# Performance work log

Measured on AMD Instinct MI355X. Metric: run time of the kernel, lower is better.

## Reference

```python
import jax, jax.numpy as jnp
import numpy as np

N, E = 50000, 1600000
DIM_IN, HEADS, DIM_OUT = 256, 4, 32
NEG_SLOPE = 0.2


def setup_inputs() -> dict:
    key = jax.random.key(0)
    k1, k2, k3, k4, k5, k6 = jax.random.split(key, 6)
    x = jax.random.normal(k1, (N, DIM_IN), dtype=jnp.float32)
    edge_index = jax.random.randint(k2, (2, E), 0, N, dtype=jnp.int64)
    s = 1.0 / np.sqrt(DIM_IN)
    W = jax.random.normal(k3, (DIM_IN, HEADS * DIM_OUT), dtype=jnp.float32) * s
    att_src = jax.random.normal(k4, (HEADS, DIM_OUT), dtype=jnp.float32) * 0.1
    att_dst = jax.random.normal(k5, (HEADS, DIM_OUT), dtype=jnp.float32) * 0.1
    bias = jax.random.normal(k6, (HEADS * DIM_OUT,), dtype=jnp.float32) * 0.01
    return {"x": x, "edge_index": edge_index, "W": W,
            "att_src": att_src, "att_dst": att_dst, "bias": bias}


def reference(x, edge_index, W, att_src, att_dst, bias):
    n = x.shape[0]
    h, c = att_src.shape
    # linear projection, per-head view [N, H, C]
    xp = (x @ W).reshape(n, h, c)
    # per-node attention logits [N, H]
    a_src = jnp.einsum('nhc,hc->nh', xp, att_src)
    a_dst = jnp.einsum('nhc,hc->nh', xp, att_dst)
    # add self loops (PyG default add_self_loops=True)
    loops = jnp.arange(n, dtype=edge_index.dtype)
    src = jnp.concatenate([edge_index[0], loops])  # [E+N]
    dst = jnp.concatenate([edge_index[1], loops])
    # edge attention scores [E+N, H]
    e = jax.nn.leaky_relu(a_src[src] + a_dst[dst], negative_slope=NEG_SLOPE)
    # segment softmax over incoming edges of each dst node
    emax = jax.ops.segment_max(e, dst, num_segments=n)
    ex = jnp.exp(e - emax[dst])
    denom = jax.ops.segment_sum(ex, dst, num_segments=n)
    alpha = ex / denom[dst]  # [E+N, H]
    # weighted scatter-aggregate of src features
    msg = xp[src] * alpha[:, :, None]  # [E+N, H, C]
    out = jax.ops.segment_sum(msg, dst, num_segments=n)  # [N, H, C]
    return out.reshape(n, h * c) + bias
```

## Files before the change

### kernel.cpp

```cpp
#include <hip/hip_runtime.h>
#include <hip/hip_fp16.h>


#define DIN 256
#define HC 128
#define NH 4
#define NEG 0.2f
#define BSH 8
#define BSZ 256

typedef _Float16 half8 __attribute__((ext_vector_type(8)));
typedef _Float16 half2v __attribute__((ext_vector_type(2)));
typedef float f32x4 __attribute__((ext_vector_type(4)));

__global__ __launch_bounds__(256) void wtrans_kernel(const float* __restrict__ W,
                                                     _Float16* __restrict__ Wt,
                                                     int* __restrict__ ghist) {
    int i = blockIdx.x * 256 + threadIdx.x;
    if (i < 257) ghist[i] = 0;
    int k = i >> 7, c = i & 127;
    Wt[c * 256 + k] = (_Float16)W[i];
}

__global__ __launch_bounds__(256) void proj_kernel(const float* __restrict__ x,
                                                   const _Float16* __restrict__ Wt,
                                                   const float* __restrict__ attS,
                                                   const float* __restrict__ attD,
                                                   __half* __restrict__ xph,
                                                   float* __restrict__ a_src,
                                                   float* __restrict__ a_dst, int n) {
    __shared__ _Float16 smem[8704];
    __shared__ float attSL[128], attDL[128];
    _Float16* xs = smem;
    _Float16* Wl = smem + 2560;
    _Float16* ep = smem;

    const int tid  = threadIdx.x;
    const int node0 = blockIdx.x * 64;
    const int wave = tid >> 6;
    const int lane = tid & 63;
    const int l15  = lane & 15;
    const int quad = lane >> 4;

    if (tid < 128) attSL[tid] = attS[tid];
    else           attDL[tid - 128] = attD[tid - 128];

    f32x4 acc[8];
#pragma unroll
    for (int ct = 0; ct < 8; ++ct) acc[ct] = (f32x4){0.f, 0.f, 0.f, 0.f};

    for (int kt = 0; kt < DIN; kt += 32) {
        __syncthreads();
#pragma unroll
        for (int r = 0; r < 4; ++r) {
            int idx = tid + r * 256;
            int row = idx >> 4;
            int kp  = idx & 15;
            int gn = node0 + row;
            float2 xv = make_float2(0.f, 0.f);
            if (gn < n) xv = *(const float2*)&x[(size_t)gn * DIN + kt + kp * 2];
            half2v p; p[0] = (_Float16)xv.x; p[1] = (_Float16)xv.y;
            *(half2v*)&xs[row * 40 + kp * 2] = p;
        }
#pragma unroll
        for (int r = 0; r < 2; ++r) {
            int id = tid + r * 256;
            int c = id >> 2;
            int q = id & 3;
            half8 wv = *(const half8*)&Wt[(size_t)c * 256 + kt + q * 8];
            *(half8*)&Wl[c * 40 + q * 8] = wv;
        }
        __syncthreads();
        half8 af = *(const half8*)&xs[(wave * 16 + l15) * 40 + quad * 8];
#pragma unroll
        for (int ct = 0; ct < 8; ++ct) {
            half8 bf = *(const half8*)&Wl[(ct * 16 + l15) * 40 + quad * 8];
            acc[ct] = __builtin_amdgcn_mfma_f32_16x16x32_f16(af, bf, acc[ct], 0, 0, 0);
        }
    }
    __syncthreads();
#pragma unroll
    for (int ct = 0; ct < 8; ++ct)
#pragma unroll
        for (int r = 0; r < 4; ++r) {
            int row = wave * 16 + quad * 4 + r;
            ep[row * 136 + ct * 16 + l15] = (_Float16)acc[ct][r];
        }
    __syncthreads();
    {
        int row = tid >> 2, ch = tid & 3;
        int node = node0 + row;
        if (node < n) {
            const uint4* s = (const uint4*)&ep[row * 136 + ch * 32];
            uint4* d = (uint4*)&xph[(size_t)node * HC + ch * 32];
            d[0] = s[0]; d[1] = s[1]; d[2] = s[2]; d[3] = s[3];
        }
    }
    {
        int nl = tid >> 2, h = tid & 3;
        int node = node0 + nl;
        if (node < n) {
            float ps = 0.f, pd = 0.f;
            const _Float16* er = &ep[nl * 136 + h * 32];
#pragma unroll
            for (int c = 0; c < 32; ++c) {
                float v = (float)er[c];
                ps += v * attSL[h * 32 + c];
                pd += v * attDL[h * 32 + c];
            }
            a_src[node * NH + h] = ps;
            a_dst[node * NH + h] = pd;
        }
    }
}

__global__ __launch_bounds__(256) void hist_kernel(const int* __restrict__ ei,
                                                   int* __restrict__ ghist, int e, int n) {
    __shared__ int h[256];
    const int tid = threadIdx.x;
    h[tid] = 0;
    __syncthreads();
    const int base = blockIdx.x * 4096;
#pragma unroll
    for (int j = 0; j < 16; ++j) {
        int i = base + j * 256 + tid;
        if (i < e) {
            int dst = ei[e + i];
            if ((unsigned)dst < (unsigned)n) atomicAdd(&h[dst >> BSH], 1);
        }
    }
    __syncthreads();
    if (h[tid]) atomicAdd(&ghist[tid], h[tid]);
}

__global__ __launch_bounds__(256) void bscan_kernel(const int* __restrict__ ghist,
                                                    int* __restrict__ gbase,
                                                    int* __restrict__ gcur, int nbuck) {
    __shared__ int buf[256];
    const int tid = threadIdx.x;
    int v = (tid < nbuck) ? ghist[tid] : 0;
    buf[tid] = v;
    __syncthreads();
    for (int s = 1; s < 256; s <<= 1) {
        int t = (tid >= s) ? buf[tid - s] : 0;
        __syncthreads();
        buf[tid] += t;
        __syncthreads();
    }
    int excl = buf[tid] - v;
    if (tid < nbuck) { gbase[tid] = excl; gcur[tid] = excl; }
    if (tid == nbuck - 1) gbase[nbuck] = buf[tid];
}

__global__ __launch_bounds__(256) void bin_kernel(const int* __restrict__ ei,
                                                  int* __restrict__ gcur,
                                                  unsigned* __restrict__ binned,
                                                  int e, int n) {
    __shared__ int h[256];
    __shared__ int rbase[256];
    const int tid = threadIdx.x;
    h[tid] = 0;
    __syncthreads();
    const int base = blockIdx.x * 4096;
    unsigned pk[16];
    int bk[16];
#pragma unroll
    for (int j = 0; j < 16; ++j) {
        int i = base + j * 256 + tid;
        bk[j] = -1;
        if (i < e) {
            int src = ei[i];
            int dst = ei[e + i];
            if ((unsigned)dst < (unsigned)n && (unsigned)src < (unsigned)n) {
                bk[j] = dst >> BSH;
                pk[j] = ((unsigned)(dst & (BSZ - 1)) << 24) | (unsigned)src;
                atomicAdd(&h[bk[j]], 1);
            }
        }
    }
    __syncthreads();
    if (h[tid]) rbase[tid] = atomicAdd(&gcur[tid], h[tid]);
    h[tid] = 0;
    __syncthreads();
#pragma unroll
    for (int j = 0; j < 16; ++j) {
        if (bk[j] >= 0) {
            int p = atomicAdd(&h[bk[j]], 1);
            binned[rbase[bk[j]] + p] = pk[j];
        }
    }
}

__global__ __launch_bounds__(1024) void csr_kernel(const unsigned* __restrict__ binned,
                                                   const int* __restrict__ gbase,
                                                   int* __restrict__ off,
                                                   unsigned* __restrict__ srt,
                                                   int n, int nbuck) {
    __shared__ int cnt[256], buf[256], cur[256];
    const int tid = threadIdx.x;
    const int b = blockIdx.x;
    const int kb = gbase[b];
    const int ke = gbase[b + 1];
    if (tid < 256) cnt[tid] = 0;
    __syncthreads();
    for (int i = kb + tid; i < ke; i += 1024)
        atomicAdd(&cnt[binned[i] >> 24], 1);
    __syncthreads();
    int v = 0;
    if (tid < 256) { v = cnt[tid]; buf[tid] = v; }
    __syncthreads();
    for (int s = 1; s < 256; s <<= 1) {
        int t = (tid < 256 && tid >= s) ? buf[tid - s] : 0;
        __syncthreads();
        if (tid < 256) buf[tid] += t;
        __syncthreads();
    }
    if (tid < 256) {
        const int excl = kb + buf[tid] - v;
        const int node = b * BSZ + tid;
        if (node < n) off[node] = excl;
        if (tid == 0 && b == nbuck - 1) off[n] = ke;
        cur[tid] = excl;
    }
    __syncthreads();
    const unsigned dbase = (unsigned)(b * BSZ) << 16;
    for (int i = kb + tid; i < ke; i += 1024) {
        unsigned pv = binned[i];
        int nl = pv >> 24;
        int pos = atomicAdd(&cur[nl], 1);
        srt[pos] = (dbase + ((unsigned)nl << 16)) | (pv & 0xFFFFu);
    }
}

__global__ __launch_bounds__(256) void escore_kernel(const unsigned* __restrict__ srt,
                                                     const float* __restrict__ a_src,
                                                     const float* __restrict__ a_dst,
                                                     __half* __restrict__ escore,
                                                     int e, int n) {
    int i = blockIdx.x * 256 + threadIdx.x;
    if (i >= e) return;
    unsigned v = srt[i];
    int src = (int)(v & 0xFFFFu);
    int dst = (int)(v >> 16);
    if (src >= n || dst >= n) return;
    const float4 as = *(const float4*)&a_src[(size_t)src * 4];
    const float4 ad = *(const float4*)&a_dst[(size_t)dst * 4];
    float t0 = as.x + ad.x; t0 = (t0 > 0.f) ? t0 : NEG * t0;
    float t1 = as.y + ad.y; t1 = (t1 > 0.f) ? t1 : NEG * t1;
    float t2 = as.z + ad.z; t2 = (t2 > 0.f) ? t2 : NEG * t2;
    float t3 = as.w + ad.w; t3 = (t3 > 0.f) ? t3 : NEG * t3;
    __half2* ep = (__half2*)&escore[(size_t)i * 4];
    ep[0] = __floats2half2_rn(__expf(t0), __expf(t1));
    ep[1] = __floats2half2_rn(__expf(t2), __expf(t3));
}

__global__ __launch_bounds__(256) void agg_kernel(const __half* __restrict__ xph,
                                                  const float* __restrict__ a_src,
                                                  const float* __restrict__ a_dst,
                                                  const int* __restrict__ off,
                                                  const unsigned* __restrict__ srt,
                                                  const __half* __restrict__ escore,
                                                  const float* __restrict__ bias,
                                                  float* __restrict__ out, int n) {
    const int gwave = (blockIdx.x * blockDim.x + threadIdx.x) >> 6;
    if (gwave >= n) return;
    const int node = gwave;
    const int lane = threadIdx.x & 63;
    const int g = lane >> 4;
    const int l = lane & 15;
    const int h = l >> 2;

    float acc[8];
#pragma unroll
    for (int c = 0; c < 8; ++c) acc[c] = 0.f;
    float den = 0.f;

    if (g == 0) {
        float e0 = a_src[node * NH + h] + a_dst[node * NH + h];
        e0 = (e0 > 0.f) ? e0 : NEG * e0;
        float sl = __expf(e0);
        half8 xv = *(const half8*)&xph[(size_t)node * HC + l * 8];
#pragma unroll
        for (int c = 0; c < 8; ++c) acc[c] = sl * (float)xv[c];
        den = sl;
    }

    const int kb = off[node];
    const int ke = off[node + 1];
    int k0 = kb;
    for (; k0 + 16 <= ke; k0 += 16) {
        const int kg = k0 + g * 4;
        unsigned sv[4];
        float sc[4];
        half8 hv[4];
#pragma unroll
        for (int j = 0; j < 4; ++j) sv[j] = srt[kg + j];
#pragma unroll
        for (int j = 0; j < 4; ++j)
            hv[j] = *(const half8*)&xph[(size_t)(sv[j] & 0xFFFFu) * HC + l * 8];
#pragma unroll
        for (int j = 0; j < 4; ++j)
            sc[j] = __half2float(escore[(size_t)(kg + j) * 4 + h]);
#pragma unroll
        for (int j = 0; j < 4; ++j) {
            const float s = sc[j];
#pragma unroll
            for (int c = 0; c < 8; ++c) acc[c] += s * (float)hv[j][c];
            den += s;
        }
    }
    for (int k = k0 + g; k < ke; k += 4) {
        const unsigned v = srt[k];
        const float s = __half2float(escore[(size_t)k * 4 + h]);
        const half8 hv = *(const half8*)&xph[(size_t)(v & 0xFFFFu) * HC + l * 8];
#pragma unroll
        for (int c = 0; c < 8; ++c) acc[c] += s * (float)hv[c];
        den += s;
    }

#pragma unroll
    for (int c = 0; c < 8; ++c) acc[c] += __shfl_xor(acc[c], 16, 64);
    den += __shfl_xor(den, 16, 64);
#pragma unroll
    for (int c = 0; c < 8; ++c) acc[c] += __shfl_xor(acc[c], 32, 64);
    den += __shfl_xor(den, 32, 64);

    if (lane < 16) {
        const float inv = 1.0f / den;
        const float4* b4 = (const float4*)&bias[l * 8];
        float4 o0, o1;
        o0.x = acc[0] * inv + b4[0].x;
        o0.y = acc[1] * inv + b4[0].y;
        o0.z = acc[2] * inv + b4[0].z;
        o0.w = acc[3] * inv + b4[0].w;
        o1.x = acc[4] * inv + b4[1].x;
        o1.y = acc[5] * inv + b4[1].y;
        o1.z = acc[6] * inv + b4[1].z;
        o1.w = acc[7] * inv + b4[1].w;
        float4* d = (float4*)&out[(size_t)node * HC + l * 8];
        d[0] = o0;
        d[1] = o1;
    }
}

extern "C" void kernel_launch(void* const* d_in, const int* in_sizes, int n_in,
                              void* d_out, int out_size, void* d_ws, size_t ws_size,
                              hipStream_t stream) {
    if (n_in < 6 || !d_out || !d_ws) return;
    const float* x    = (const float*)d_in[0];
    const int*   ei   = (const int*)d_in[1];
    const float* W    = (const float*)d_in[2];
    const float* attS = (const float*)d_in[3];
    const float* attD = (const float*)d_in[4];
    const float* bias = (const float*)d_in[5];
    float* out = (float*)d_out;

    const int N = in_sizes[0] / DIN;
    const int E = in_sizes[1] / 2;
    if (N <= 0 || E <= 0) return;
    const int NBUCK = (N + BSZ - 1) >> BSH;
    if (NBUCK > 256 || N > 65536) return;

    char* ws = (char*)d_ws;
    size_t off_b = 0;
    auto carve = [&](size_t bytes) {
        size_t p = off_b;
        off_b = (off_b + bytes + 255) & ~(size_t)255;
        return (void*)(ws + p);
    };
    __half*    xph    = (__half*)carve((size_t)N * HC * 2);
    _Float16*  Wt     = (_Float16*)carve((size_t)HC * DIN * 2);
    float*     a_src  = (float*)carve((size_t)N * NH * 4);
    float*     a_dst  = (float*)carve((size_t)N * NH * 4);
    int*       ghist  = (int*)carve(257 * 4);
    int*       gbase  = (int*)carve(257 * 4);
    int*       gcur   = (int*)carve(257 * 4);
    unsigned*  binned = (unsigned*)carve((size_t)E * 4);
    int*       offp   = (int*)carve((size_t)(N + 1) * 4);
    unsigned*  srt    = (unsigned*)carve((size_t)E * 4);
    __half*    escore = (__half*)carve((size_t)E * NH * 2);
    (void)out_size;
    if (off_b > ws_size) return;

    const int ECH = (E + 4095) / 4096;

    wtrans_kernel<<<(DIN * HC) / 256, 256, 0, stream>>>(W, Wt, ghist);
    proj_kernel<<<(N + 63) / 64, 256, 0, stream>>>(x, Wt, attS, attD, (__half*)xph, a_src, a_dst, N);
    hist_kernel<<<ECH, 256, 0, stream>>>(ei, ghist, E, N);
    bscan_kernel<<<1, 256, 0, stream>>>(ghist, gbase, gcur, NBUCK);
    bin_kernel<<<ECH, 256, 0, stream>>>(ei, gcur, binned, E, N);
    csr_kernel<<<NBUCK, 1024, 0, stream>>>(binned, gbase, offp, srt, N, NBUCK);
    escore_kernel<<<(E + 255) / 256, 256, 0, stream>>>(srt, a_src, a_dst, escore, E, N);
    agg_kernel<<<(N * 64 + 255) / 256, 256, 0, stream>>>(xph, a_src, a_dst,
                                                         offp, srt, escore, bias, out, N);
}
```

Baseline: 240.6 us.

## Merge preprocessing kernels, overlap projection with binning, recompute edge scores in aggregation

Cuts the kernel chain from eight launches to five. Histogram runs alongside the weight transpose, the bucket scan is recomputed per block instead of in its own launch, and the projection is split across the binning and CSR launches so independent work shares the GPU. The separate edge-score kernel and its fp16 escore buffer are gone: aggregation now gathers a_src per edge and computes exp(leaky_relu) inline. The sorted index array shrinks to 16-bit source ids. This trades redundant per-block scans and extra gathers and exp work in aggregation for fewer launches and less global memory traffic.

New measurement: 233.4 us. 1.03x faster.

```diff
diff --git a/kernel.cpp b/kernel.cpp
--- a/kernel.cpp
+++ b/kernel.cpp
@@ -13,30 +13,25 @@
 typedef _Float16 half2v __attribute__((ext_vector_type(2)));
 typedef float f32x4 __attribute__((ext_vector_type(4)));
 
-__global__ __launch_bounds__(256) void wtrans_kernel(const float* __restrict__ W,
-                                                     _Float16* __restrict__ Wt,
-                                                     int* __restrict__ ghist) {
-    int i = blockIdx.x * 256 + threadIdx.x;
-    if (i < 257) ghist[i] = 0;
-    int k = i >> 7, c = i & 127;
-    Wt[c * 256 + k] = (_Float16)W[i];
-}
-
-__global__ __launch_bounds__(256) void proj_kernel(const float* __restrict__ x,
-                                                   const _Float16* __restrict__ Wt,
-                                                   const float* __restrict__ attS,
-                                                   const float* __restrict__ attD,
-                                                   __half* __restrict__ xph,
-                                                   float* __restrict__ a_src,
-                                                   float* __restrict__ a_dst, int n) {
-    __shared__ _Float16 smem[8704];
-    __shared__ float attSL[128], attDL[128];
-    _Float16* xs = smem;
-    _Float16* Wl = smem + 2560;
-    _Float16* ep = smem;
+__global__ void zero_kernel(int* __restrict__ p, int n) {
+    int i = blockIdx.x * blockDim.x + threadIdx.x;
+    if (i < n) p[i] = 0;
+}
+
+__device__ __forceinline__ void proj_body(char* sm, const float* __restrict__ x,
+                                          const _Float16* __restrict__ Wt,
+                                          const float* __restrict__ attS,
+                                          const float* __restrict__ attD,
+                                          __half* __restrict__ xph,
+                                          float* __restrict__ a_src,
+                                          float* __restrict__ a_dst, int n, int node0) {
+    _Float16* xs = (_Float16*)sm;
+    _Float16* Wl = (_Float16*)(sm + 5120);
+    _Float16* ep = (_Float16*)sm;
+    float* attSL = (float*)(sm + 17408);
+    float* attDL = (float*)(sm + 17920);
 
     const int tid  = threadIdx.x;
-    const int node0 = blockIdx.x * 64;
     const int wave = tid >> 6;
     const int lane = tid & 63;
     const int l15  = lane & 15;
@@ -114,152 +109,163 @@
     }
 }
 
-__global__ __launch_bounds__(256) void hist_kernel(const int* __restrict__ ei,
-                                                   int* __restrict__ ghist, int e, int n) {
-    __shared__ int h[256];
-    const int tid = threadIdx.x;
-    h[tid] = 0;
-    __syncthreads();
-    const int base = blockIdx.x * 4096;
-#pragma unroll
-    for (int j = 0; j < 16; ++j) {
-        int i = base + j * 256 + tid;
-        if (i < e) {
-            int dst = ei[e + i];
-            if ((unsigned)dst < (unsigned)n) atomicAdd(&h[dst >> BSH], 1);
-        }
-    }
-    __syncthreads();
-    if (h[tid]) atomicAdd(&ghist[tid], h[tid]);
-}
-
-__global__ __launch_bounds__(256) void bscan_kernel(const int* __restrict__ ghist,
-                                                    int* __restrict__ gbase,
-                                                    int* __restrict__ gcur, int nbuck) {
-    __shared__ int buf[256];
-    const int tid = threadIdx.x;
-    int v = (tid < nbuck) ? ghist[tid] : 0;
-    buf[tid] = v;
-    __syncthreads();
-    for (int s = 1; s < 256; s <<= 1) {
-        int t = (tid >= s) ? buf[tid - s] : 0;
-        __syncthreads();
-        buf[tid] += t;
-        __syncthreads();
-    }
-    int excl = buf[tid] - v;
-    if (tid < nbuck) { gbase[tid] = excl; gcur[tid] = excl; }
-    if (tid == nbuck - 1) gbase[nbuck] = buf[tid];
-}
-
-__global__ __launch_bounds__(256) void bin_kernel(const int* __restrict__ ei,
-                                                  int* __restrict__ gcur,
+__global__ __launch_bounds__(256) void k_hist_wtrans(const int* __restrict__ ei,
+                                                     int* __restrict__ ghist,
+                                                     const float* __restrict__ W,
+                                                     _Float16* __restrict__ Wt,
+                                                     int e, int n, int ech) {
+    if ((int)blockIdx.x < ech) {
+        __shared__ int h[256];
+        const int tid = threadIdx.x;
+        h[tid] = 0;
+        __syncthreads();
+        const int base = blockIdx.x * 4096;
+#pragma unroll
+        for (int j = 0; j < 16; ++j) {
+            int i = base + j * 256 + tid;
+            if (i < e) {
+                int dst = ei[e + i];
+                if ((unsigned)dst < (unsigned)n) atomicAdd(&h[dst >> BSH], 1);
+            }
+        }
+        __syncthreads();
+        if (h[tid]) atomicAdd(&ghist[tid], h[tid]);
+    } else {
+        int i = ((int)blockIdx.x - ech) * 256 + threadIdx.x;
+        int k = i >> 7, c = i & 127;
+        Wt[c * 256 + k] = (_Float16)W[i];
+    }
+}
+
+__global__ __launch_bounds__(256) void k_bin_proj(const int* __restrict__ ei,
+                                                  const int* __restrict__ ghist,
+                                                  int* __restrict__ gcur0,
                                                   unsigned* __restrict__ binned,
-                                                  int e, int n) {
-    __shared__ int h[256];
-    __shared__ int rbase[256];
-    const int tid = threadIdx.x;
-    h[tid] = 0;
-    __syncthreads();
-    const int base = blockIdx.x * 4096;
-    unsigned pk[16];
-    int bk[16];
-#pragma unroll
-    for (int j = 0; j < 16; ++j) {
-        int i = base + j * 256 + tid;
-        bk[j] = -1;
-        if (i < e) {
-            int src = ei[i];
-            int dst = ei[e + i];
-            if ((unsigned)dst < (unsigned)n && (unsigned)src < (unsigned)n) {
-                bk[j] = dst >> BSH;
-                pk[j] = ((unsigned)(dst & (BSZ - 1)) << 24) | (unsigned)src;
-                atomicAdd(&h[bk[j]], 1);
+                                                  const float* __restrict__ x,
+                                                  const _Float16* __restrict__ Wt,
+                                                  const float* __restrict__ attS,
+                                                  const float* __restrict__ attD,
+                                                  __half* __restrict__ xph,
+                                                  float* __restrict__ a_src,
+                                                  float* __restrict__ a_dst,
+                                                  int e, int n, int ech) {
+    __shared__ __attribute__((aligned(16))) char sm[18432];
+    if ((int)blockIdx.x < ech) {
+        int* h     = (int*)sm;
+        int* rbase = (int*)(sm + 1024);
+        int* buf   = (int*)(sm + 2048);
+        const int tid = threadIdx.x;
+        const int gh = ghist[tid];
+        buf[tid] = gh;
+        h[tid] = 0;
+        __syncthreads();
+        for (int s = 1; s < 256; s <<= 1) {
+            int t = (tid >= s) ? buf[tid - s] : 0;
+            __syncthreads();
+            buf[tid] += t;
+            __syncthreads();
+        }
+        const int gbase_t = buf[tid] - gh;
+        const int base = blockIdx.x * 4096;
+        unsigned pk[16];
+        int bk[16];
+#pragma unroll
+        for (int j = 0; j < 16; ++j) {
+            int i = base + j * 256 + tid;
+            bk[j] = -1;
+            if (i < e) {
+                int src = ei[i];
+                int dst = ei[e + i];
+                if ((unsigned)dst < (unsigned)n && (unsigned)src < (unsigned)n) {
+                    bk[j] = dst >> BSH;
+                    pk[j] = ((unsigned)(dst & (BSZ - 1)) << 24) | (unsigned)src;
+                    atomicAdd(&h[bk[j]], 1);
+                }
             }
         }
-    }
-    __syncthreads();
-    if (h[tid]) rbase[tid] = atomicAdd(&gcur[tid], h[tid]);
-    h[tid] = 0;
-    __syncthreads();
-#pragma unroll
-    for (int j = 0; j < 16; ++j) {
-        if (bk[j] >= 0) {
-            int p = atomicAdd(&h[bk[j]], 1);
-            binned[rbase[bk[j]] + p] = pk[j];
-        }
-    }
-}
-
-__global__ __launch_bounds__(1024) void csr_kernel(const unsigned* __restrict__ binned,
-                                                   const int* __restrict__ gbase,
-                                                   int* __restrict__ off,
-                                                   unsigned* __restrict__ srt,
-                                                   int n, int nbuck) {
-    __shared__ int cnt[256], buf[256], cur[256];
-    const int tid = threadIdx.x;
-    const int b = blockIdx.x;
-    const int kb = gbase[b];
-    const int ke = gbase[b + 1];
-    if (tid < 256) cnt[tid] = 0;
-    __syncthreads();
-    for (int i = kb + tid; i < ke; i += 1024)
-        atomicAdd(&cnt[binned[i] >> 24], 1);
-    __syncthreads();
-    int v = 0;
-    if (tid < 256) { v = cnt[tid]; buf[tid] = v; }
-    __syncthreads();
-    for (int s = 1; s < 256; s <<= 1) {
-        int t = (tid < 256 && tid >= s) ? buf[tid - s] : 0;
-        __syncthreads();
-        if (tid < 256) buf[tid] += t;
-        __syncthreads();
-    }
-    if (tid < 256) {
+        __syncthreads();
+        if (h[tid]) rbase[tid] = gbase_t + atomicAdd(&gcur0[tid], h[tid]);
+        h[tid] = 0;
+        __syncthreads();
+#pragma unroll
+        for (int j = 0; j < 16; ++j) {
+            if (bk[j] >= 0) {
+                int p = atomicAdd(&h[bk[j]], 1);
+                binned[rbase[bk[j]] + p] = pk[j];
+            }
+        }
+    } else {
+        proj_body(sm, x, Wt, attS, attD, xph, a_src, a_dst, n, ((int)blockIdx.x - ech) * 64);
+    }
+}
+
+__global__ __launch_bounds__(256) void k_csr_proj(const unsigned* __restrict__ binned,
+                                                  const int* __restrict__ ghist,
+                                                  int* __restrict__ off,
+                                                  unsigned short* __restrict__ srt,
+                                                  const float* __restrict__ x,
+                                                  const _Float16* __restrict__ Wt,
+                                                  const float* __restrict__ attS,
+                                                  const float* __restrict__ attD,
+                                                  __half* __restrict__ xph,
+                                                  float* __restrict__ a_src,
+                                                  float* __restrict__ a_dst,
+                                                  int n, int nbuck, int pb1) {
+    __shared__ __attribute__((aligned(16))) char sm[18432];
+    if ((int)blockIdx.x < nbuck) {
+        int* cnt = (int*)sm;
+        int* buf = (int*)(sm + 1024);
+        int* cur = (int*)(sm + 2048);
+        const int tid = threadIdx.x;
+        const int b = blockIdx.x;
+        buf[tid] = ghist[tid];
+        __syncthreads();
+        for (int s = 1; s < 256; s <<= 1) {
+            int t = (tid >= s) ? buf[tid - s] : 0;
+            __syncthreads();
+            buf[tid] += t;
+            __syncthreads();
+        }
+        const int ke = buf[b];
+        const int kb = ke - ghist[b];
+        __syncthreads();
+        cnt[tid] = 0;
+        __syncthreads();
+        for (int i = kb + tid; i < ke; i += 256)
+            atomicAdd(&cnt[binned[i] >> 24], 1);
+        __syncthreads();
+        int v = cnt[tid];
+        buf[tid] = v;
+        __syncthreads();
+        for (int s = 1; s < 256; s <<= 1) {
+            int t = (tid >= s) ? buf[tid - s] : 0;
+            __syncthreads();
+            buf[tid] += t;
+            __syncthreads();
+        }
         const int excl = kb + buf[tid] - v;
         const int node = b * BSZ + tid;
         if (node < n) off[node] = excl;
         if (tid == 0 && b == nbuck - 1) off[n] = ke;
         cur[tid] = excl;
-    }
-    __syncthreads();
-    const unsigned dbase = (unsigned)(b * BSZ) << 16;
-    for (int i = kb + tid; i < ke; i += 1024) {
-        unsigned pv = binned[i];
-        int nl = pv >> 24;
-        int pos = atomicAdd(&cur[nl], 1);
-        srt[pos] = (dbase + ((unsigned)nl << 16)) | (pv & 0xFFFFu);
-    }
-}
-
-__global__ __launch_bounds__(256) void escore_kernel(const unsigned* __restrict__ srt,
-                                                     const float* __restrict__ a_src,
-                                                     const float* __restrict__ a_dst,
-                                                     __half* __restrict__ escore,
-                                                     int e, int n) {
-    int i = blockIdx.x * 256 + threadIdx.x;
-    if (i >= e) return;
-    unsigned v = srt[i];
-    int src = (int)(v & 0xFFFFu);
-    int dst = (int)(v >> 16);
-    if (src >= n || dst >= n) return;
-    const float4 as = *(const float4*)&a_src[(size_t)src * 4];
-    const float4 ad = *(const float4*)&a_dst[(size_t)dst * 4];
-    float t0 = as.x + ad.x; t0 = (t0 > 0.f) ? t0 : NEG * t0;
-    float t1 = as.y + ad.y; t1 = (t1 > 0.f) ? t1 : NEG * t1;
-    float t2 = as.z + ad.z; t2 = (t2 > 0.f) ? t2 : NEG * t2;
-    float t3 = as.w + ad.w; t3 = (t3 > 0.f) ? t3 : NEG * t3;
-    __half2* ep = (__half2*)&escore[(size_t)i * 4];
-    ep[0] = __floats2half2_rn(__expf(t0), __expf(t1));
-    ep[1] = __floats2half2_rn(__expf(t2), __expf(t3));
+        __syncthreads();
+        for (int i = kb + tid; i < ke; i += 256) {
+            unsigned pv = binned[i];
+            int nl = pv >> 24;
+            int pos = atomicAdd(&cur[nl], 1);
+            srt[pos] = (unsigned short)(pv & 0xFFFFu);
+        }
+    } else {
+        proj_body(sm, x, Wt, attS, attD, xph, a_src, a_dst, n,
+                  (pb1 + (int)blockIdx.x - nbuck) * 64);
+    }
 }
 
 __global__ __launch_bounds__(256) void agg_kernel(const __half* __restrict__ xph,
                                                   const float* __restrict__ a_src,
                                                   const float* __restrict__ a_dst,
                                                   const int* __restrict__ off,
-                                                  const unsigned* __restrict__ srt,
-                                                  const __half* __restrict__ escore,
+                                                  const unsigned short* __restrict__ srt,
                                                   const float* __restrict__ bias,
                                                   float* __restrict__ out, int n) {
     const int gwave = (blockIdx.x * blockDim.x + threadIdx.x) >> 6;
@@ -270,19 +276,21 @@
     const int l = lane & 15;
     const int h = l >> 2;
 
+    const float ad = a_dst[node * NH + h];
+
     float acc[8];
 #pragma unroll
     for (int c = 0; c < 8; ++c) acc[c] = 0.f;
     float den = 0.f;
 
     if (g == 0) {
-        float e0 = a_src[node * NH + h] + a_dst[node * NH + h];
-        e0 = (e0 > 0.f) ? e0 : NEG * e0;
-        float sl = __expf(e0);
+        float t = a_src[node * NH + h] + ad;
+        t = fmaxf(t, 0.f) + NEG * fminf(t, 0.f);
+        float s = __expf(t);
         half8 xv = *(const half8*)&xph[(size_t)node * HC + l * 8];
 #pragma unroll
-        for (int c = 0; c < 8; ++c) acc[c] = sl * (float)xv[c];
-        den = sl;
+        for (int c = 0; c < 8; ++c) acc[c] = s * (float)xv[c];
+        den = s;
     }
 
     const int kb = off[node];
@@ -290,29 +298,32 @@
     int k0 = kb;
     for (; k0 + 16 <= ke; k0 += 16) {
         const int kg = k0 + g * 4;
-        unsigned sv[4];
-        float sc[4];
+        int sv[4];
+        float asv[4];
         half8 hv[4];
 #pragma unroll
         for (int j = 0; j < 4; ++j) sv[j] = srt[kg + j];
 #pragma unroll
+        for (int j = 0; j < 4; ++j) asv[j] = a_src[sv[j] * NH + h];
+#pragma unroll
         for (int j = 0; j < 4; ++j)
-            hv[j] = *(const half8*)&xph[(size_t)(sv[j] & 0xFFFFu) * HC + l * 8];
-#pragma unroll
-        for (int j = 0; j < 4; ++j)
-            sc[j] = __half2float(escore[(size_t)(kg + j) * 4 + h]);
+            hv[j] = *(const half8*)&xph[(size_t)sv[j] * HC + l * 8];
 #pragma unroll
         for (int j = 0; j < 4; ++j) {
-            const float s = sc[j];
+            float t = asv[j] + ad;
+            t = fmaxf(t, 0.f) + NEG * fminf(t, 0.f);
+            const float s = __expf(t);
 #pragma unroll
             for (int c = 0; c < 8; ++c) acc[c] += s * (float)hv[j][c];
             den += s;
         }
     }
     for (int k = k0 + g; k < ke; k += 4) {
-        const unsigned v = srt[k];
-        const float s = __half2float(escore[(size_t)k * 4 + h]);
-        const half8 hv = *(const half8*)&xph[(size_t)(v & 0xFFFFu) * HC + l * 8];
+        const int sv = srt[k];
+        float t = a_src[sv * NH + h] + ad;
+        t = fmaxf(t, 0.f) + NEG * fminf(t, 0.f);
+        const float s = __expf(t);
+        const half8 hv = *(const half8*)&xph[(size_t)sv * HC + l * 8];
 #pragma unroll
         for (int c = 0; c < 8; ++c) acc[c] += s * (float)hv[c];
         den += s;
@@ -368,29 +379,32 @@
         off_b = (off_b + bytes + 255) & ~(size_t)255;
         return (void*)(ws + p);
     };
-    __half*    xph    = (__half*)carve((size_t)N * HC * 2);
-    _Float16*  Wt     = (_Float16*)carve((size_t)HC * DIN * 2);
-    float*     a_src  = (float*)carve((size_t)N * NH * 4);
-    float*     a_dst  = (float*)carve((size_t)N * NH * 4);
-    int*       ghist  = (int*)carve(257 * 4);
-    int*       gbase  = (int*)carve(257 * 4);
-    int*       gcur   = (int*)carve(257 * 4);
-    unsigned*  binned = (unsigned*)carve((size_t)E * 4);
-    int*       offp   = (int*)carve((size_t)(N + 1) * 4);
-    unsigned*  srt    = (unsigned*)carve((size_t)E * 4);
-    __half*    escore = (__half*)carve((size_t)E * NH * 2);
+    __half*         xph    = (__half*)carve((size_t)N * HC * 2);
+    _Float16*       Wt     = (_Float16*)carve((size_t)HC * DIN * 2);
+    float*          a_src  = (float*)carve((size_t)N * NH * 4);
+    float*          a_dst  = (float*)carve((size_t)N * NH * 4);
+    int*            gz     = (int*)carve(512 * 4);
+    unsigned*       binned = (unsigned*)carve((size_t)E * 4);
+    int*            offp   = (int*)carve((size_t)(N + 1) * 4);
+    unsigned short* srt    = (unsigned short*)carve((size_t)E * 2);
     (void)out_size;
     if (off_b > ws_size) return;
 
+    int* ghist = gz;
+    int* gcur0 = gz + 256;
+
     const int ECH = (E + 4095) / 4096;
-
-    wtrans_kernel<<<(DIN * HC) / 256, 256, 0, stream>>>(W, Wt, ghist);
-    proj_kernel<<<(N + 63) / 64, 256, 0, stream>>>(x, Wt, attS, attD, (__half*)xph, a_src, a_dst, N);
-    hist_kernel<<<ECH, 256, 0, stream>>>(ei, ghist, E, N);
-    bscan_kernel<<<1, 256, 0, stream>>>(ghist, gbase, gcur, NBUCK);
-    bin_kernel<<<ECH, 256, 0, stream>>>(ei, gcur, binned, E, N);
-    csr_kernel<<<NBUCK, 1024, 0, stream>>>(binned, gbase, offp, srt, N, NBUCK);
-    escore_kernel<<<(E + 255) / 256, 256, 0, stream>>>(srt, a_src, a_dst, escore, E, N);
+    const int PB  = (N + 63) / 64;
+    const int PB1 = PB / 2;
+
+    zero_kernel<<<2, 256, 0, stream>>>(gz, 512);
+    k_hist_wtrans<<<ECH + 128, 256, 0, stream>>>(ei, ghist, W, Wt, E, N, ECH);
+    k_bin_proj<<<ECH + PB1, 256, 0, stream>>>(ei, ghist, gcur0, binned,
+                                              x, Wt, attS, attD, xph, a_src, a_dst,
+                                              E, N, ECH);
+    k_csr_proj<<<NBUCK + (PB - PB1), 256, 0, stream>>>(binned, ghist, offp, srt,
+                                                       x, Wt, attS, attD, xph, a_src, a_dst,
+                                                       N, NBUCK, PB1);
     agg_kernel<<<(N * 64 + 255) / 256, 256, 0, stream>>>(xph, a_src, a_dst,
-                                                         offp, srt, escore, bias, out, N);
-}
+                                                         offp, srt, bias, out, N);
+}
```
